# Kernel tuning notes

Measured on AMD Instinct MI355X. Metric: run time of the kernel, lower is better.

## Reference

```python
import jax, jax.numpy as jnp
import numpy as np

B, C, H, W = 4, 64, 64, 64
E = C // 8  # embedding_channels = inChannels // k


def _conv1x1(x, w, b):
    # x:[B,C,H,W], w:[O,C], b:[O] -> [B,O,H,W]
    return jnp.einsum('bchw,oc->bohw', x, w) + b[None, :, None, None]


def setup_inputs() -> dict:
    key = jax.random.key(0)
    ks = jax.random.split(key, 10)
    s_c = 1.0 / np.sqrt(C)
    s_e = 1.0 / np.sqrt(E)
    x = jax.random.normal(ks[0], (B, C, H, W), jnp.float32)
    Wk = jax.random.normal(ks[1], (E, C), jnp.float32) * s_c
    bk = jax.random.normal(ks[2], (E,), jnp.float32) * 0.01
    Wq = jax.random.normal(ks[3], (E, C), jnp.float32) * s_c
    bq = jax.random.normal(ks[4], (E,), jnp.float32) * 0.01
    Wv = jax.random.normal(ks[5], (E, C), jnp.float32) * s_c
    bv = jax.random.normal(ks[6], (E,), jnp.float32) * 0.01
    Wo = jax.random.normal(ks[7], (C, E), jnp.float32) * s_e
    bo = jax.random.normal(ks[8], (C,), jnp.float32) * 0.01
    gamma = jax.random.normal(ks[9], (), jnp.float32) * 0.1  # module inits to 0; randomized for nontrivial math
    return {"x": x, "Wk": Wk, "bk": bk, "Wq": Wq, "bq": bq,
            "Wv": Wv, "bv": bv, "Wo": Wo, "bo": bo, "gamma": gamma}


def reference(x, Wk, bk, Wq, bq, Wv, bv, Wo, bo, gamma):
    b, c, h, w = x.shape
    n = h * w
    f = _conv1x1(x, Wk, bk).reshape(b, E, n)  # key
    g = _conv1x1(x, Wq, bq).reshape(b, E, n)  # query
    hx = _conv1x1(x, Wv, bv).reshape(b, E, n)  # value
    # s[b,i,j] = sum_e f[b,e,i] * g[b,e,j]  (bmm(f^T, g))
    s = jnp.einsum('bei,bej->bij', f, g)
    # torch softmax over dim=1 (the f/key index i)
    beta = jax.nn.softmax(s, axis=1)
    # v[b,e,j] = sum_i hx[b,e,i] * beta[b,i,j]
    v = jnp.einsum('bei,bij->bej', hx, beta).reshape(b, E, h, w)
    o = _conv1x1(v, Wo, bo)
    y = gamma * o + x
    y = jnp.where(y >= 0, y, 0.01 * y)  # LeakyReLU(0.01)
    return (y, beta)
```

## Files before the change

### kernel.cpp

```cpp
#include <hip/hip_runtime.h>


namespace {
constexpr int Bb = 4;
constexpr int Cc = 64;
constexpr int Nn = 4096;
constexpr int Ee = 8;
constexpr int COLS = 64;
constexpr int SPLIT = 4;
constexpr int CHUNK = Nn / SPLIT;
constexpr int W2 = 8;
constexpr int IS2 = CHUNK / W2;
constexpr float LOG2E = 1.4426950408889634f;
}

#if defined(__has_builtin)
#if __has_builtin(__builtin_amdgcn_exp2f)
#define EXP2F(x) __builtin_amdgcn_exp2f(x)
#endif
#endif
#ifndef EXP2F
#define EXP2F(x) exp2f(x)
#endif

__global__ __launch_bounds__(256) void proj_kernel(
    const float* __restrict__ x,
    const float* __restrict__ Wk, const float* __restrict__ bk,
    const float* __restrict__ Wq, const float* __restrict__ bq,
    const float* __restrict__ Wv, const float* __restrict__ bv,
    float* __restrict__ fo, float* __restrict__ go, float* __restrict__ ho)
{
    __shared__ float wk[Ee * Cc], wq[Ee * Cc], wv[Ee * Cc];
    __shared__ float sb[3 * Ee];
    const int t = threadIdx.x;
    for (int i = t; i < Ee * Cc; i += 256) { wk[i] = Wk[i]; wq[i] = Wq[i]; wv[i] = Wv[i]; }
    if (t < Ee) { sb[t] = bk[t]; sb[Ee + t] = bq[t]; sb[2 * Ee + t] = bv[t]; }
    __syncthreads();

    const int gidx = blockIdx.x * 256 + t;
    const int b = gidx >> 12;
    const int n = gidx & (Nn - 1);

    float af[Ee], ag[Ee], ah[Ee];
#pragma unroll
    for (int e = 0; e < Ee; e++) { af[e] = sb[e]; ag[e] = sb[Ee + e]; ah[e] = sb[2 * Ee + e]; }

    const float* xp = x + (size_t)b * Cc * Nn + n;
#pragma unroll 4
    for (int c = 0; c < Cc; c++) {
        const float xv = xp[(size_t)c * Nn];
#pragma unroll
        for (int e = 0; e < Ee; e++) {
            af[e] = fmaf(wk[e * Cc + c], xv, af[e]);
            ag[e] = fmaf(wq[e * Cc + c], xv, ag[e]);
            ah[e] = fmaf(wv[e * Cc + c], xv, ah[e]);
        }
    }
    float4* fp = (float4*)(fo + (size_t)gidx * Ee);
    float4* gp = (float4*)(go + (size_t)gidx * Ee);
    float4* hp = (float4*)(ho + (size_t)gidx * Ee);
    fp[0] = make_float4(af[0], af[1], af[2], af[3]);
    fp[1] = make_float4(af[4], af[5], af[6], af[7]);
    gp[0] = make_float4(ag[0], ag[1], ag[2], ag[3]);
    gp[1] = make_float4(ag[4], ag[5], ag[6], ag[7]);
    hp[0] = make_float4(ah[0], ah[1], ah[2], ah[3]);
    hp[1] = make_float4(ah[4], ah[5], ah[6], ah[7]);
}

__global__ __launch_bounds__(512, 8) void sums_kernel(
    const float* __restrict__ f, const float* __restrict__ g,
    float* __restrict__ sums_part)
{
    const int b = blockIdx.x >> 8;
    const int jbase = ((blockIdx.x >> 2) & 63) * COLS;
    const int si = blockIdx.x & 3;
    const int t = threadIdx.x;
    const int lane = t & 63;
    const int w = __builtin_amdgcn_readfirstlane(t >> 6);
    const int j = jbase + lane;

    const float4* gp = (const float4*)(g + ((size_t)b * Nn + j) * Ee);
    const float4 g0 = gp[0], g1 = gp[1];
    const float gq[Ee] = {g0.x * LOG2E, g0.y * LOG2E, g0.z * LOG2E, g0.w * LOG2E,
                          g1.x * LOG2E, g1.y * LOG2E, g1.z * LOG2E, g1.w * LOG2E};

    const float* fb = f + (size_t)b * Nn * Ee;
    const int i0 = si * CHUNK + w * IS2;

    float sum = 0.f;
#pragma unroll 4
    for (int ii = 0; ii < IS2; ii++) {
        const float4* fr = (const float4*)(fb + (size_t)(i0 + ii) * Ee);
        const float4 a0 = fr[0], a1 = fr[1];
        float sA = a0.x * gq[0];
        sA = fmaf(a0.y, gq[1], sA); sA = fmaf(a0.z, gq[2], sA); sA = fmaf(a0.w, gq[3], sA);
        float sB = a1.x * gq[4];
        sB = fmaf(a1.y, gq[5], sB); sB = fmaf(a1.z, gq[6], sB); sB = fmaf(a1.w, gq[7], sB);
        sum += EXP2F(sA + sB);
    }
    __shared__ float red[W2][COLS];
    red[w][lane] = sum;
    __syncthreads();
    if (t < COLS) {
        float sf = 0.f;
#pragma unroll
        for (int ww = 0; ww < W2; ww++) sf += red[ww][t];
        sums_part[(size_t)si * (Bb * Nn) + (size_t)b * Nn + jbase + t] = sf;
    }
}

__global__ __launch_bounds__(512, 4) void beta_kernel(
    const float* __restrict__ f, const float* __restrict__ g,
    const float* __restrict__ h, const float* __restrict__ sums_part,
    float* __restrict__ beta, float* __restrict__ v_part)
{
    const int b = blockIdx.x >> 8;
    const int jbase = ((blockIdx.x >> 2) & 63) * COLS;
    const int si = blockIdx.x & 3;
    const int t = threadIdx.x;
    const int lane = t & 63;
    const int w = __builtin_amdgcn_readfirstlane(t >> 6);
    const int j = jbase + lane;

    const float4* gp = (const float4*)(g + ((size_t)b * Nn + j) * Ee);
    const float4 g0 = gp[0], g1 = gp[1];
    const float gq[Ee] = {g0.x * LOG2E, g0.y * LOG2E, g0.z * LOG2E, g0.w * LOG2E,
                          g1.x * LOG2E, g1.y * LOG2E, g1.z * LOG2E, g1.w * LOG2E};

    float sf = 0.f;
#pragma unroll
    for (int s2 = 0; s2 < SPLIT; s2++)
        sf += sums_part[(size_t)s2 * (Bb * Nn) + (size_t)b * Nn + j];
    const float inv = 1.0f / sf;

    const float* fb = f + (size_t)b * Nn * Ee;
    const float* hb = h + (size_t)b * Nn * Ee;
    const int i0 = si * CHUNK + w * IS2;

    float vacc[Ee] = {0.f, 0.f, 0.f, 0.f, 0.f, 0.f, 0.f, 0.f};
    float* bp = beta + (size_t)b * Nn * Nn + (size_t)jbase + lane;
#pragma unroll 4
    for (int ii = 0; ii < IS2; ii++) {
        const int i = i0 + ii;
        const float4* fr = (const float4*)(fb + (size_t)i * Ee);
        const float4 a0 = fr[0], a1 = fr[1];
        float sA = a0.x * gq[0];
        sA = fmaf(a0.y, gq[1], sA); sA = fmaf(a0.z, gq[2], sA); sA = fmaf(a0.w, gq[3], sA);
        float sB = a1.x * gq[4];
        sB = fmaf(a1.y, gq[5], sB); sB = fmaf(a1.z, gq[6], sB); sB = fmaf(a1.w, gq[7], sB);
        const float p = EXP2F(sA + sB) * inv;
        __builtin_nontemporal_store(p, bp + (size_t)i * Nn);
        const float4* hr = (const float4*)(hb + (size_t)i * Ee);
        const float4 h0 = hr[0], h1 = hr[1];
        vacc[0] = fmaf(h0.x, p, vacc[0]); vacc[1] = fmaf(h0.y, p, vacc[1]);
        vacc[2] = fmaf(h0.z, p, vacc[2]); vacc[3] = fmaf(h0.w, p, vacc[3]);
        vacc[4] = fmaf(h1.x, p, vacc[4]); vacc[5] = fmaf(h1.y, p, vacc[5]);
        vacc[6] = fmaf(h1.z, p, vacc[6]); vacc[7] = fmaf(h1.w, p, vacc[7]);
    }

    __shared__ float vred[W2][COLS][Ee];
    float4* vw = (float4*)&vred[w][lane][0];
    vw[0] = make_float4(vacc[0], vacc[1], vacc[2], vacc[3]);
    vw[1] = make_float4(vacc[4], vacc[5], vacc[6], vacc[7]);
    __syncthreads();
    {
        const int col = t >> 3;
        const int e = t & 7;
        float acc = 0.f;
#pragma unroll
        for (int ww = 0; ww < W2; ww++) acc += vred[ww][col][e];
        v_part[(size_t)si * (Bb * Nn * Ee) +
               ((size_t)b * Nn + jbase + col) * Ee + e] = acc;
    }
}

__global__ __launch_bounds__(256) void out_kernel(
    const float* __restrict__ v_part, const float* __restrict__ Wo,
    const float* __restrict__ bo, const float* __restrict__ x,
    const float* __restrict__ gamma_p, float* __restrict__ y)
{
    __shared__ float wo[Cc * Ee];
    __shared__ float sbo[Cc];
    const int t = threadIdx.x;
    for (int i = t; i < Cc * Ee; i += 256) wo[i] = Wo[i];
    if (t < Cc) sbo[t] = bo[t];
    __syncthreads();
    const float gamma = gamma_p[0];

    const int gidx = blockIdx.x * 256 + t;
    const int b = gidx >> 12;
    const int n = gidx & (Nn - 1);

    float vv[Ee] = {0.f, 0.f, 0.f, 0.f, 0.f, 0.f, 0.f, 0.f};
#pragma unroll
    for (int si = 0; si < SPLIT; si++) {
        const float4* vp = (const float4*)(v_part + (size_t)si * (Bb * Nn * Ee) + (size_t)gidx * Ee);
        const float4 v0 = vp[0], v1 = vp[1];
        vv[0] += v0.x; vv[1] += v0.y; vv[2] += v0.z; vv[3] += v0.w;
        vv[4] += v1.x; vv[5] += v1.y; vv[6] += v1.z; vv[7] += v1.w;
    }

    const float* xp = x + (size_t)b * Cc * Nn + n;
    float* yp = y + (size_t)b * Cc * Nn + n;
#pragma unroll 4
    for (int c = 0; c < Cc; c++) {
        float o = sbo[c];
#pragma unroll
        for (int e = 0; e < Ee; e++) o = fmaf(wo[c * Ee + e], vv[e], o);
        const float t2 = fmaf(gamma, o, xp[(size_t)c * Nn]);
        yp[(size_t)c * Nn] = (t2 >= 0.f) ? t2 : 0.01f * t2;
    }
}

extern "C" void kernel_launch(void* const* d_in, const int* in_sizes, int n_in,
                              void* d_out, int out_size, void* d_ws, size_t ws_size,
                              hipStream_t stream)
{
    const float* x     = (const float*)d_in[0];
    const float* Wk    = (const float*)d_in[1];
    const float* bk    = (const float*)d_in[2];
    const float* Wq    = (const float*)d_in[3];
    const float* bq    = (const float*)d_in[4];
    const float* Wv    = (const float*)d_in[5];
    const float* bv    = (const float*)d_in[6];
    const float* Wo    = (const float*)d_in[7];
    const float* bo    = (const float*)d_in[8];
    const float* gamma = (const float*)d_in[9];

    float* y    = (float*)d_out;
    float* beta = y + (size_t)Bb * Cc * Nn;

    float* f = (float*)d_ws;
    float* g = f + (size_t)Bb * Nn * Ee;
    float* h = g + (size_t)Bb * Nn * Ee;
    float* sums_part = h + (size_t)Bb * Nn * Ee;
    float* v_part = sums_part + (size_t)SPLIT * Bb * Nn;

    const int grid2 = Bb * (Nn / COLS) * SPLIT;

    proj_kernel<<<Bb * Nn / 256, 256, 0, stream>>>(x, Wk, bk, Wq, bq, Wv, bv, f, g, h);
    sums_kernel<<<grid2, W2 * 64, 0, stream>>>(f, g, sums_part);
    beta_kernel<<<grid2, W2 * 64, 0, stream>>>(f, g, h, sums_part, beta, v_part);
    out_kernel<<<Bb * Nn / 256, 256, 0, stream>>>(v_part, Wo, bo, x, gamma, y);
}
```

Before: 347.2 us.

## Restructure beta kernel: 4 columns per thread, vector stores, atomic v reduction

```diff
diff --git a/kernel.cpp b/kernel.cpp
--- a/kernel.cpp
+++ b/kernel.cpp
@@ -7,12 +7,20 @@
 constexpr int Nn = 4096;
 constexpr int Ee = 8;
 constexpr int COLS = 64;
-constexpr int SPLIT = 4;
-constexpr int CHUNK = Nn / SPLIT;
-constexpr int W2 = 8;
-constexpr int IS2 = CHUNK / W2;
+constexpr int SPLIT_B = 4;
+constexpr int CHUNK_B = Nn / SPLIT_B;
+constexpr int WB = 8;
+constexpr int ISB = CHUNK_B / WB;
+constexpr int VPT = 4;
+constexpr int TC = 256;
+constexpr int JW = TC * VPT;
+constexpr int JGROUPS = Nn / JW;
+constexpr int SC = 32;
+constexpr int IC = Nn / SC;
 constexpr float LOG2E = 1.4426950408889634f;
 }
+
+typedef float f4v __attribute__((ext_vector_type(4)));
 
 #if defined(__has_builtin)
 #if __has_builtin(__builtin_amdgcn_exp2f)
@@ -28,7 +36,8 @@
     const float* __restrict__ Wk, const float* __restrict__ bk,
     const float* __restrict__ Wq, const float* __restrict__ bq,
     const float* __restrict__ Wv, const float* __restrict__ bv,
-    float* __restrict__ fo, float* __restrict__ go, float* __restrict__ ho)
+    float* __restrict__ fo, float* __restrict__ go, float* __restrict__ ho,
+    float* __restrict__ v_zero)
 {
     __shared__ float wk[Ee * Cc], wq[Ee * Cc], wv[Ee * Cc];
     __shared__ float sb[3 * Ee];
@@ -40,6 +49,10 @@
     const int gidx = blockIdx.x * 256 + t;
     const int b = gidx >> 12;
     const int n = gidx & (Nn - 1);
+
+    float4* vz = (float4*)(v_zero + (size_t)gidx * Ee);
+    vz[0] = make_float4(0.f, 0.f, 0.f, 0.f);
+    vz[1] = make_float4(0.f, 0.f, 0.f, 0.f);
 
     float af[Ee], ag[Ee], ah[Ee];
 #pragma unroll
@@ -85,11 +98,11 @@
                           g1.x * LOG2E, g1.y * LOG2E, g1.z * LOG2E, g1.w * LOG2E};
 
     const float* fb = f + (size_t)b * Nn * Ee;
-    const int i0 = si * CHUNK + w * IS2;
+    const int i0 = si * CHUNK_B + w * ISB;
 
     float sum = 0.f;
 #pragma unroll 4
-    for (int ii = 0; ii < IS2; ii++) {
+    for (int ii = 0; ii < ISB; ii++) {
         const float4* fr = (const float4*)(fb + (size_t)(i0 + ii) * Ee);
         const float4 a0 = fr[0], a1 = fr[1];
         float sA = a0.x * gq[0];
@@ -98,84 +111,104 @@
         sB = fmaf(a1.y, gq[5], sB); sB = fmaf(a1.z, gq[6], sB); sB = fmaf(a1.w, gq[7], sB);
         sum += EXP2F(sA + sB);
     }
-    __shared__ float red[W2][COLS];
+    __shared__ float red[WB][COLS];
     red[w][lane] = sum;
     __syncthreads();
     if (t < COLS) {
         float sf = 0.f;
 #pragma unroll
-        for (int ww = 0; ww < W2; ww++) sf += red[ww][t];
+        for (int ww = 0; ww < WB; ww++) sf += red[ww][t];
         sums_part[(size_t)si * (Bb * Nn) + (size_t)b * Nn + jbase + t] = sf;
     }
 }
 
-__global__ __launch_bounds__(512, 4) void beta_kernel(
+__global__ __launch_bounds__(TC, 4) void beta_kernel(
     const float* __restrict__ f, const float* __restrict__ g,
     const float* __restrict__ h, const float* __restrict__ sums_part,
-    float* __restrict__ beta, float* __restrict__ v_part)
-{
-    const int b = blockIdx.x >> 8;
-    const int jbase = ((blockIdx.x >> 2) & 63) * COLS;
-    const int si = blockIdx.x & 3;
-    const int t = threadIdx.x;
-    const int lane = t & 63;
-    const int w = __builtin_amdgcn_readfirstlane(t >> 6);
-    const int j = jbase + lane;
-
-    const float4* gp = (const float4*)(g + ((size_t)b * Nn + j) * Ee);
-    const float4 g0 = gp[0], g1 = gp[1];
-    const float gq[Ee] = {g0.x * LOG2E, g0.y * LOG2E, g0.z * LOG2E, g0.w * LOG2E,
-                          g1.x * LOG2E, g1.y * LOG2E, g1.z * LOG2E, g1.w * LOG2E};
-
-    float sf = 0.f;
-#pragma unroll
-    for (int s2 = 0; s2 < SPLIT; s2++)
-        sf += sums_part[(size_t)s2 * (Bb * Nn) + (size_t)b * Nn + j];
-    const float inv = 1.0f / sf;
+    float* __restrict__ beta, float* __restrict__ v_out)
+{
+    const int blk = blockIdx.x;
+    const int b  = blk >> 7;
+    const int jg = (blk >> 5) & (JGROUPS - 1);
+    const int s  = blk & (SC - 1);
+    const int t  = threadIdx.x;
+    const int j0 = jg * JW + t * VPT;
+
+    float gq[VPT][Ee];
+    {
+        const float* gp = g + ((size_t)b * Nn + j0) * Ee;
+#pragma unroll
+        for (int jj = 0; jj < VPT; jj++) {
+            const float4 a0 = ((const float4*)(gp + jj * Ee))[0];
+            const float4 a1 = ((const float4*)(gp + jj * Ee))[1];
+            gq[jj][0] = a0.x * LOG2E; gq[jj][1] = a0.y * LOG2E;
+            gq[jj][2] = a0.z * LOG2E; gq[jj][3] = a0.w * LOG2E;
+            gq[jj][4] = a1.x * LOG2E; gq[jj][5] = a1.y * LOG2E;
+            gq[jj][6] = a1.z * LOG2E; gq[jj][7] = a1.w * LOG2E;
+        }
+    }
+
+    float inv[VPT];
+#pragma unroll
+    for (int jj = 0; jj < VPT; jj++) {
+        float sf = 0.f;
+#pragma unroll
+        for (int s2 = 0; s2 < SPLIT_B; s2++)
+            sf += sums_part[(size_t)s2 * (Bb * Nn) + (size_t)b * Nn + j0 + jj];
+        inv[jj] = 1.0f / sf;
+    }
 
     const float* fb = f + (size_t)b * Nn * Ee;
     const float* hb = h + (size_t)b * Nn * Ee;
-    const int i0 = si * CHUNK + w * IS2;
-
-    float vacc[Ee] = {0.f, 0.f, 0.f, 0.f, 0.f, 0.f, 0.f, 0.f};
-    float* bp = beta + (size_t)b * Nn * Nn + (size_t)jbase + lane;
-#pragma unroll 4
-    for (int ii = 0; ii < IS2; ii++) {
+    float vacc[VPT][Ee] = {};
+    float* bp = beta + (size_t)b * Nn * Nn + j0;
+    const int i0 = s * IC;
+
+    for (int ii = 0; ii < IC; ii++) {
         const int i = i0 + ii;
-        const float4* fr = (const float4*)(fb + (size_t)i * Ee);
-        const float4 a0 = fr[0], a1 = fr[1];
-        float sA = a0.x * gq[0];
-        sA = fmaf(a0.y, gq[1], sA); sA = fmaf(a0.z, gq[2], sA); sA = fmaf(a0.w, gq[3], sA);
-        float sB = a1.x * gq[4];
-        sB = fmaf(a1.y, gq[5], sB); sB = fmaf(a1.z, gq[6], sB); sB = fmaf(a1.w, gq[7], sB);
-        const float p = EXP2F(sA + sB) * inv;
-        __builtin_nontemporal_store(p, bp + (size_t)i * Nn);
-        const float4* hr = (const float4*)(hb + (size_t)i * Ee);
-        const float4 h0 = hr[0], h1 = hr[1];
-        vacc[0] = fmaf(h0.x, p, vacc[0]); vacc[1] = fmaf(h0.y, p, vacc[1]);
-        vacc[2] = fmaf(h0.z, p, vacc[2]); vacc[3] = fmaf(h0.w, p, vacc[3]);
-        vacc[4] = fmaf(h1.x, p, vacc[4]); vacc[5] = fmaf(h1.y, p, vacc[5]);
-        vacc[6] = fmaf(h1.z, p, vacc[6]); vacc[7] = fmaf(h1.w, p, vacc[7]);
-    }
-
-    __shared__ float vred[W2][COLS][Ee];
-    float4* vw = (float4*)&vred[w][lane][0];
-    vw[0] = make_float4(vacc[0], vacc[1], vacc[2], vacc[3]);
-    vw[1] = make_float4(vacc[4], vacc[5], vacc[6], vacc[7]);
-    __syncthreads();
-    {
-        const int col = t >> 3;
-        const int e = t & 7;
-        float acc = 0.f;
-#pragma unroll
-        for (int ww = 0; ww < W2; ww++) acc += vred[ww][col][e];
-        v_part[(size_t)si * (Bb * Nn * Ee) +
-               ((size_t)b * Nn + jbase + col) * Ee + e] = acc;
-    }
+        const float4 a0 = ((const float4*)(fb + (size_t)i * Ee))[0];
+        const float4 a1 = ((const float4*)(fb + (size_t)i * Ee))[1];
+        const float4 h0 = ((const float4*)(hb + (size_t)i * Ee))[0];
+        const float4 h1 = ((const float4*)(hb + (size_t)i * Ee))[1];
+        float p[VPT];
+#pragma unroll
+        for (int jj = 0; jj < VPT; jj++) {
+            float sA = a0.x * gq[jj][0];
+            sA = fmaf(a0.y, gq[jj][1], sA);
+            sA = fmaf(a0.z, gq[jj][2], sA);
+            sA = fmaf(a0.w, gq[jj][3], sA);
+            float sB = a1.x * gq[jj][4];
+            sB = fmaf(a1.y, gq[jj][5], sB);
+            sB = fmaf(a1.z, gq[jj][6], sB);
+            sB = fmaf(a1.w, gq[jj][7], sB);
+            p[jj] = EXP2F(sA + sB) * inv[jj];
+        }
+        f4v pv = {p[0], p[1], p[2], p[3]};
+        __builtin_nontemporal_store(pv, (f4v*)(bp + (size_t)i * Nn));
+#pragma unroll
+        for (int jj = 0; jj < VPT; jj++) {
+            const float pj = p[jj];
+            vacc[jj][0] = fmaf(h0.x, pj, vacc[jj][0]);
+            vacc[jj][1] = fmaf(h0.y, pj, vacc[jj][1]);
+            vacc[jj][2] = fmaf(h0.z, pj, vacc[jj][2]);
+            vacc[jj][3] = fmaf(h0.w, pj, vacc[jj][3]);
+            vacc[jj][4] = fmaf(h1.x, pj, vacc[jj][4]);
+            vacc[jj][5] = fmaf(h1.y, pj, vacc[jj][5]);
+            vacc[jj][6] = fmaf(h1.z, pj, vacc[jj][6]);
+            vacc[jj][7] = fmaf(h1.w, pj, vacc[jj][7]);
+        }
+    }
+
+    float* vp = v_out + ((size_t)b * Nn + j0) * Ee;
+#pragma unroll
+    for (int jj = 0; jj < VPT; jj++)
+#pragma unroll
+        for (int e = 0; e < Ee; e++)
+            atomicAdd(vp + jj * Ee + e, vacc[jj][e]);
 }
 
 __global__ __launch_bounds__(256) void out_kernel(
-    const float* __restrict__ v_part, const float* __restrict__ Wo,
+    const float* __restrict__ v, const float* __restrict__ Wo,
     const float* __restrict__ bo, const float* __restrict__ x,
     const float* __restrict__ gamma_p, float* __restrict__ y)
 {
@@ -191,14 +224,9 @@
     const int b = gidx >> 12;
     const int n = gidx & (Nn - 1);
 
-    float vv[Ee] = {0.f, 0.f, 0.f, 0.f, 0.f, 0.f, 0.f, 0.f};
-#pragma unroll
-    for (int si = 0; si < SPLIT; si++) {
-        const float4* vp = (const float4*)(v_part + (size_t)si * (Bb * Nn * Ee) + (size_t)gidx * Ee);
-        const float4 v0 = vp[0], v1 = vp[1];
-        vv[0] += v0.x; vv[1] += v0.y; vv[2] += v0.z; vv[3] += v0.w;
-        vv[4] += v1.x; vv[5] += v1.y; vv[6] += v1.z; vv[7] += v1.w;
-    }
+    const float4* vp = (const float4*)(v + (size_t)gidx * Ee);
+    const float4 v0 = vp[0], v1 = vp[1];
+    const float vv[Ee] = {v0.x, v0.y, v0.z, v0.w, v1.x, v1.y, v1.z, v1.w};
 
     const float* xp = x + (size_t)b * Cc * Nn + n;
     float* yp = y + (size_t)b * Cc * Nn + n;
@@ -234,12 +262,10 @@
     float* g = f + (size_t)Bb * Nn * Ee;
     float* h = g + (size_t)Bb * Nn * Ee;
     float* sums_part = h + (size_t)Bb * Nn * Ee;
-    float* v_part = sums_part + (size_t)SPLIT * Bb * Nn;
-
-    const int grid2 = Bb * (Nn / COLS) * SPLIT;
-
-    proj_kernel<<<Bb * Nn / 256, 256, 0, stream>>>(x, Wk, bk, Wq, bq, Wv, bv, f, g, h);
-    sums_kernel<<<grid2, W2 * 64, 0, stream>>>(f, g, sums_part);
-    beta_kernel<<<grid2, W2 * 64, 0, stream>>>(f, g, h, sums_part, beta, v_part);
-    out_kernel<<<Bb * Nn / 256, 256, 0, stream>>>(v_part, Wo, bo, x, gamma, y);
-}
+    float* v = sums_part + (size_t)SPLIT_B * Bb * Nn;
+
+    proj_kernel<<<Bb * Nn / 256, 256, 0, stream>>>(x, Wk, bk, Wq, bq, Wv, bv, f, g, h, v);
+    sums_kernel<<<Bb * (Nn / COLS) * SPLIT_B, 512, 0, stream>>>(f, g, sums_part);
+    beta_kernel<<<Bb * JGROUPS * SC, TC, 0, stream>>>(f, g, h, sums_part, beta, v);
+    out_kernel<<<Bb * Nn / 256, 256, 0, stream>>>(v, Wo, bo, x, gamma, y);
+}
```

Result: slower. 545.9 us (+57.2%).
